# Optimization experiments

Hardware: AMD Instinct MI355X
Metric: run time of the kernel (lower is better)

Reference implementation:

```python
import jax, jax.numpy as jnp
import numpy as np

H, D_MODEL, D_K, D_V = 16, 1024, 64, 64
IS_DECODE = True


def setup_inputs() -> dict:
    key = jax.random.key(0)
    ks = jax.random.split(key, 6)
    N, L = 4, 2048
    x = jax.random.normal(ks[0], (N, L, D_MODEL), dtype=jnp.float32)
    masked_info = jnp.ones((N, L), dtype=jnp.float32)  # 1 = valid, 0 = pad
    s = 1.0 / np.sqrt(D_MODEL)
    WQ = jax.random.normal(ks[1], (H, D_MODEL, D_K), dtype=jnp.float32) * s
    WK = jax.random.normal(ks[2], (H, D_MODEL, D_K), dtype=jnp.float32) * s
    WV = jax.random.normal(ks[3], (H, D_MODEL, D_V), dtype=jnp.float32) * s
    WO = jax.random.normal(ks[4], (H * D_V, D_MODEL), dtype=jnp.float32) * s
    return {"x": x, "masked_info": masked_info, "WQ": WQ, "WK": WK, "WV": WV, "WO": WO}


def reference(x, masked_info, WQ, WK, WV, WO):
    N, L, _ = x.shape
    scaler = jnp.sqrt(jnp.array(D_K, dtype=x.dtype))
    # per-head projections, batched over heads: [H, N, L, d]
    q = jnp.einsum('nld,hdk->hnlk', x, WQ)
    k = jnp.einsum('nld,hdk->hnlk', x, WK)
    v = jnp.einsum('nld,hdv->hnlv', x, WV)
    scores = jnp.einsum('hnlk,hnmk->hnlm', q, k) / scaler  # [H, N, L, L]
    # outer-product padding mask: True where masked out
    pad_mask = (masked_info[:, :, None] * masked_info[:, None, :]) == 0  # [N, L, L]
    if IS_DECODE:
        causal = jnp.triu(jnp.ones((L, L), dtype=bool), k=1)
        pad_mask = pad_mask | causal[None, :, :]
    scores = jnp.where(pad_mask[None], -jnp.inf, scores)
    attn = jax.nn.softmax(scores, axis=-1)
    attn = jnp.nan_to_num(attn, nan=0.0)  # rows fully masked -> 0
    out_h = jnp.einsum('hnlm,hnmv->hnlv', attn, v)  # [H, N, L, d_v]
    # concat heads along last dim in head order: [N, L, H*d_v]
    concat = jnp.transpose(out_h, (1, 2, 0, 3)).reshape(N, L, H * D_V)
    return concat @ WO
```

## Files before the change

kernel.cpp:

```cpp
#include <hip/hip_runtime.h>
#include <hip/hip_bf16.h>


typedef unsigned short ushort_t;
typedef __bf16 bf16x8 __attribute__((ext_vector_type(8)));
typedef float  f32x4  __attribute__((ext_vector_type(4)));
typedef unsigned short us4 __attribute__((ext_vector_type(4)));
typedef short s16x4 __attribute__((ext_vector_type(4)));

__device__ __forceinline__ ushort_t f2bf(float f) {
    union { float f; unsigned u; } a; a.f = f;
    unsigned r = a.u + 0x7fffu + ((a.u >> 16) & 1u);
    return (ushort_t)(r >> 16);
}

__device__ __forceinline__ void gload16(const ushort_t* g, ushort_t* l) {
    __builtin_amdgcn_global_load_lds(
        (const __attribute__((address_space(1))) void*)g,
        (__attribute__((address_space(3))) void*)l, 16, 0, 0);
}

__global__ __launch_bounds__(256) void cvt_f32_bf16(const float* __restrict__ in,
                                                    ushort_t* __restrict__ out, int n4) {
    int i = blockIdx.x * 256 + threadIdx.x;
    if (i >= n4) return;
    float4 v = reinterpret_cast<const float4*>(in)[i];
    us4 o;
    o[0] = f2bf(v.x); o[1] = f2bf(v.y); o[2] = f2bf(v.z); o[3] = f2bf(v.w);
    reinterpret_cast<us4*>(out)[i] = o;
}

__global__ __launch_bounds__(256) void cvt_transpose32(const float* __restrict__ in,
                                                       ushort_t* __restrict__ out,
                                                       int R, int C) {
    const int b = blockIdx.z;
    const int c0 = blockIdx.x * 32, r0 = blockIdx.y * 32;
    const int tx = threadIdx.x & 31, ty = threadIdx.x >> 5;
    __shared__ ushort_t t[32][33];
    const float* ip = in + ((size_t)b * R + r0) * C + c0;
    #pragma unroll
    for (int i = 0; i < 4; ++i)
        t[ty + 8 * i][tx] = f2bf(ip[(size_t)(ty + 8 * i) * C + tx]);
    __syncthreads();
    ushort_t* op = out + ((size_t)b * C + c0) * R + r0;
    #pragma unroll
    for (int i = 0; i < 4; ++i)
        op[(size_t)(ty + 8 * i) * R + tx] = t[tx][ty + 8 * i];
}

__global__ __launch_bounds__(256) void cvt_transpose_qkv(const float* __restrict__ WQ,
                                                         const float* __restrict__ WK,
                                                         const float* __restrict__ WV,
                                                         ushort_t* __restrict__ out) {
    const int z = blockIdx.z;
    const float* in = (z < 16) ? WQ : (z < 32) ? WK : WV;
    const int b = z & 15;
    const int c0 = blockIdx.x * 32, r0 = blockIdx.y * 32;
    const int tx = threadIdx.x & 31, ty = threadIdx.x >> 5;
    __shared__ ushort_t t[32][33];
    const float* ip = in + ((size_t)b * 1024 + r0) * 64 + c0;
    #pragma unroll
    for (int i = 0; i < 4; ++i)
        t[ty + 8 * i][tx] = f2bf(ip[(size_t)(ty + 8 * i) * 64 + tx]);
    __syncthreads();
    ushort_t* op = out + (size_t)z * 65536 + (size_t)c0 * 1024 + r0;
    #pragma unroll
    for (int i = 0; i < 4; ++i)
        op[(size_t)(ty + 8 * i) * 1024 + tx] = t[tx][ty + 8 * i];
}

template<int MODE>
__global__ __launch_bounds__(256, 2)
void gemm_bt(const ushort_t* __restrict__ Ag, const ushort_t* __restrict__ BT,
             void* __restrict__ Cout, float scale) {
    const int bm = blockIdx.x, by = blockIdx.y;
    const int tid = threadIdx.x;
    const int w = tid >> 6, lane = tid & 63;
    const int wr = w >> 1, wc = w & 1;
    const int g = lane >> 4, c = lane & 15;
    const int m0 = bm * 128;
    const ushort_t* Bbase = BT + (size_t)by * 131072;

    __shared__ __align__(16) ushort_t As[128 * 64];
    __shared__ __align__(16) ushort_t Bs[128 * 64];

    f32x4 acc[4][4];
    #pragma unroll
    for (int i = 0; i < 4; ++i)
        #pragma unroll
        for (int j = 0; j < 4; ++j) acc[i][j] = (f32x4){0.f, 0.f, 0.f, 0.f};

    const int rsub = (w << 3) + (lane >> 3);
    const int s8   = lane & 7;

    for (int t = 0; t < 16; ++t) {
        const int k0 = t * 64;
        #pragma unroll
        for (int is = 0; is < 4; ++is) {
            const int row = is * 32 + rsub;
            const int sg  = (s8 ^ (row & 7)) << 3;
            gload16(Ag + (size_t)(m0 + row) * 1024 + k0 + sg, &As[is * 2048 + w * 512]);
            gload16(Bbase + (size_t)row * 1024 + k0 + sg,     &Bs[is * 2048 + w * 512]);
        }
        __syncthreads();
        #pragma unroll
        for (int kk = 0; kk < 2; ++kk) {
            bf16x8 af[4], bfr[4];
            #pragma unroll
            for (int mf = 0; mf < 4; ++mf) {
                const int row = wr * 64 + mf * 16 + c;
                const int slot = (kk * 4 + g) ^ (row & 7);
                af[mf] = *reinterpret_cast<const bf16x8*>(&As[row * 64 + slot * 8]);
            }
            #pragma unroll
            for (int nf = 0; nf < 4; ++nf) {
                const int row = wc * 64 + nf * 16 + c;
                const int slot = (kk * 4 + g) ^ (row & 7);
                bfr[nf] = *reinterpret_cast<const bf16x8*>(&Bs[row * 64 + slot * 8]);
            }
            __builtin_amdgcn_s_setprio(1);
            #pragma unroll
            for (int mf = 0; mf < 4; ++mf)
                #pragma unroll
                for (int nf = 0; nf < 4; ++nf)
                    acc[mf][nf] = __builtin_amdgcn_mfma_f32_16x16x32_bf16(
                        af[mf], bfr[nf], acc[mf][nf], 0, 0, 0);
            __builtin_amdgcn_s_setprio(0);
        }
        __syncthreads();
    }

    #pragma unroll
    for (int mf = 0; mf < 4; ++mf) {
        const int mbase = m0 + wr * 64 + mf * 16 + g * 4;
        #pragma unroll
        for (int nf = 0; nf < 4; ++nf) {
            const int colG = wc * 64 + nf * 16 + c;
            if (MODE == 3) {
                const int s  = by * 2 + (colG >> 6);
                const int c2 = colG & 63;
                ushort_t* o = (ushort_t*)Cout + (size_t)s * 524288;
                if (s < 32) {
                    const float scl = (s < 16) ? scale : 1.0f;
                    #pragma unroll
                    for (int r = 0; r < 4; ++r)
                        o[(size_t)(mbase + r) * 64 + c2] = f2bf(acc[mf][nf][r] * scl);
                } else {
                    us4 pk;
                    #pragma unroll
                    for (int r = 0; r < 4; ++r) pk[r] = f2bf(acc[mf][nf][r]);
                    const int nIdx = mbase >> 11, l = mbase & 2047;
                    *reinterpret_cast<us4*>(
                        &o[(size_t)nIdx * 131072 + (size_t)c2 * 2048 + l]) = pk;
                }
            } else {
                float* o = (float*)Cout;
                #pragma unroll
                for (int r = 0; r < 4; ++r)
                    o[(size_t)(mbase + r) * 1024 + by * 128 + colG] = acc[mf][nf][r];
            }
        }
    }
}

__global__ __launch_bounds__(256, 4)
void attn_kernel(const ushort_t* __restrict__ qb, const ushort_t* __restrict__ kb,
                 const ushort_t* __restrict__ vtb, const float* __restrict__ mi,
                 ushort_t* __restrict__ cat) {
    const int bx = blockIdx.x;
    const int n = blockIdx.y, h = blockIdx.z;
    const int tid = threadIdx.x;
    const int w = tid >> 6, lane = tid & 63;
    const int g = lane >> 4, c = lane & 15;
    const int qblkA = bx, qblkB = 31 - bx;
    const int q0A = qblkA * 64 + w * 16;
    const int q0B = qblkB * 64 + w * 16;

    const ushort_t* qhn = qb  + (size_t)h * 524288 + (size_t)n * 131072;
    const ushort_t* khn = kb  + (size_t)h * 524288 + (size_t)n * 131072;
    const ushort_t* vhn = vtb + (size_t)h * 524288 + (size_t)n * 131072;
    const float*    mrow = mi + (size_t)n * 2048;

    __shared__ __align__(16) ushort_t Ks[2][64 * 64];
    __shared__ __align__(16) ushort_t Vs[2][64 * 64];

    const int rsub = (w << 3) + (lane >> 3);
    const int s8   = lane & 7;

    auto stage = [&](int jb, int b) {
        const int kbase = jb * 64;
        #pragma unroll
        for (int is = 0; is < 2; ++is) {
            const int row = is * 32 + rsub;
            const int sg  = (s8 ^ (row & 7)) << 3;
            gload16(khn + (size_t)(kbase + row) * 64 + sg, &Ks[b][is * 2048 + w * 512]);
            gload16(vhn + (size_t)row * 2048 + kbase + sg, &Vs[b][is * 2048 + w * 512]);
        }
    };

    bf16x8 qfA[2], qfB[2];
    {
        const ushort_t* qa = qhn + (size_t)(q0A + c) * 64 + g * 8;
        const ushort_t* qb2 = qhn + (size_t)(q0B + c) * 64 + g * 8;
        qfA[0] = *reinterpret_cast<const bf16x8*>(qa);
        qfA[1] = *reinterpret_cast<const bf16x8*>(qa + 32);
        qfB[0] = *reinterpret_cast<const bf16x8*>(qb2);
        qfB[1] = *reinterpret_cast<const bf16x8*>(qb2 + 32);
    }
    const float mqA = mrow[q0A + c];
    const float mqB = mrow[q0B + c];

    float mrunA = -1e30f, lrunA = 0.f, mrunB = -1e30f, lrunB = 0.f;
    f32x4 accA[4], accB[4];
    #pragma unroll
    for (int i = 0; i < 4; ++i) {
        accA[i] = (f32x4){0.f, 0.f, 0.f, 0.f};
        accB[i] = (f32x4){0.f, 0.f, 0.f, 0.f};
    }

    stage(0, 0);
    __syncthreads();
    int buf = 0;

    for (int j = 0; j <= qblkB; ++j) {
        if (j < qblkB) stage(j + 1, buf ^ 1);
        const int kbase = j * 64;
        f32x4 bias[4];
        #pragma unroll
        for (int nf = 0; nf < 4; ++nf) {
            float4 mk = *reinterpret_cast<const float4*>(&mrow[kbase + nf * 16 + g * 4]);
            bias[nf][0] = (mk.x == 0.f) ? -1e30f : 0.f;
            bias[nf][1] = (mk.y == 0.f) ? -1e30f : 0.f;
            bias[nf][2] = (mk.z == 0.f) ? -1e30f : 0.f;
            bias[nf][3] = (mk.w == 0.f) ? -1e30f : 0.f;
        }

        auto do_pass = [&](const bf16x8* qf, f32x4* acc, float& mrun, float& lrun,
                           int q0, bool diag) {
            f32x4 s[4];
            #pragma unroll
            for (int nf = 0; nf < 4; ++nf) s[nf] = (f32x4){0.f, 0.f, 0.f, 0.f};
            __builtin_amdgcn_s_setprio(1);
            #pragma unroll
            for (int kk = 0; kk < 2; ++kk)
                #pragma unroll
                for (int nf = 0; nf < 4; ++nf) {
                    const int row  = nf * 16 + c;
                    const int byte = row * 128 + (((kk * 4 + g) ^ (c & 7)) << 4);
                    bf16x8 kf = *reinterpret_cast<const bf16x8*>(
                        reinterpret_cast<const char*>(&Ks[buf][0]) + byte);
                    s[nf] = __builtin_amdgcn_mfma_f32_16x16x32_bf16(
                        kf, qf[kk], s[nf], 0, 0, 0);
                }
            __builtin_amdgcn_s_setprio(0);
            #pragma unroll
            for (int nf = 0; nf < 4; ++nf) s[nf] += bias[nf];
            if (diag) {
                const int qrow = q0 + c;
                #pragma unroll
                for (int nf = 0; nf < 4; ++nf)
                    #pragma unroll
                    for (int r = 0; r < 4; ++r)
                        if (kbase + nf * 16 + g * 4 + r > qrow) s[nf][r] = -1e30f;
            }
            float m01[4], m23[4];
            #pragma unroll
            for (int r = 0; r < 4; ++r) {
                m01[r] = fmaxf(s[0][r], s[1][r]);
                m23[r] = fmaxf(s[2][r], s[3][r]);
            }
            const float mtl = fmaxf(fmaxf(fmaxf(m01[0], m01[1]), fmaxf(m01[2], m01[3])),
                                    fmaxf(fmaxf(m23[0], m23[1]), fmaxf(m23[2], m23[3])));
            if (!__all(mtl - mrun <= 8.0f)) {
                float mt = fmaxf(mtl, __shfl_xor(mtl, 16));
                mt = fmaxf(mt, __shfl_xor(mt, 32));
                const float mnew = fmaxf(mrun, mt);
                const float sc = __builtin_amdgcn_exp2f(mrun - mnew);
                #pragma unroll
                for (int nfd = 0; nfd < 4; ++nfd)
                    #pragma unroll
                    for (int r = 0; r < 4; ++r) acc[nfd][r] *= sc;
                lrun *= sc;
                mrun = mnew;
            }
            float rs = 0.f;
            union { unsigned u[2]; s16x4 v; } pb[4];
            #pragma unroll
            for (int nf = 0; nf < 4; ++nf) {
                const float p0 = __builtin_amdgcn_exp2f(s[nf][0] - mrun);
                const float p1 = __builtin_amdgcn_exp2f(s[nf][1] - mrun);
                const float p2 = __builtin_amdgcn_exp2f(s[nf][2] - mrun);
                const float p3 = __builtin_amdgcn_exp2f(s[nf][3] - mrun);
                rs += (p0 + p1) + (p2 + p3);
                asm("v_cvt_pk_bf16_f32 %0, %1, %2" : "=v"(pb[nf].u[0]) : "v"(p0), "v"(p1));
                asm("v_cvt_pk_bf16_f32 %0, %1, %2" : "=v"(pb[nf].u[1]) : "v"(p2), "v"(p3));
            }
            lrun += rs;
            __builtin_amdgcn_s_setprio(1);
            #pragma unroll
            for (int kk = 0; kk < 4; ++kk)
                #pragma unroll
                for (int nfd = 0; nfd < 4; ++nfd) {
                    const int row   = nfd * 16 + c;
                    const int chunk = (kk * 2 + (g >> 1)) ^ (c & 7);
                    const int byt   = row * 128 + (chunk << 4) + (g & 1) * 8;
                    s16x4 vf = *reinterpret_cast<const s16x4*>(
                        reinterpret_cast<const char*>(&Vs[buf][0]) + byt);
                    acc[nfd] = __builtin_amdgcn_mfma_f32_16x16x16bf16_1k(
                        vf, pb[kk].v, acc[nfd], 0, 0, 0);
                }
            __builtin_amdgcn_s_setprio(0);
        };

        if (j <= qblkA) do_pass(qfA, accA, mrunA, lrunA, q0A, j == qblkA);
        do_pass(qfB, accB, mrunB, lrunB, q0B, j == qblkB);

        __syncthreads();
        buf ^= 1;
    }

    auto epi = [&](const f32x4* acc, float mrun, float lrun, float mq, int q0) {
        float lt = lrun;
        lt += __shfl_xor(lt, 16);
        lt += __shfl_xor(lt, 32);
        const float inv = (mq != 0.f && mrun > -1e29f && lt > 0.f)
                              ? (1.0f / lt) : 0.f;
        const size_t base = (size_t)(n * 2048 + q0 + c) * 1024 + h * 64;
        #pragma unroll
        for (int nfd = 0; nfd < 4; ++nfd) {
            us4 pk;
            #pragma unroll
            for (int r = 0; r < 4; ++r) pk[r] = f2bf(acc[nfd][r] * inv);
            *reinterpret_cast<us4*>(&cat[base + nfd * 16 + g * 4]) = pk;
        }
    };
    epi(accA, mrunA, lrunA, mqA, q0A);
    epi(accB, mrunB, lrunB, mqB, q0B);
}

extern "C" void kernel_launch(void* const* d_in, const int* in_sizes, int n_in,
                              void* d_out, int out_size, void* d_ws, size_t ws_size,
                              hipStream_t stream) {
    const float* x  = (const float*)d_in[0];
    const float* mi = (const float*)d_in[1];
    const float* WQ = (const float*)d_in[2];
    const float* WK = (const float*)d_in[3];
    const float* WV = (const float*)d_in[4];
    const float* WO = (const float*)d_in[5];
    float* out = (float*)d_out;

    ushort_t* ws  = (ushort_t*)d_ws;
    ushort_t* xb  = ws;
    ushort_t* wqt = xb  + 8388608;
    ushort_t* wot = wqt + 3145728;
    ushort_t* qb  = wot + 1048576;
    ushort_t* kb  = qb  + 8388608;
    ushort_t* vtb = kb  + 8388608;
    ushort_t* cat = xb;

    cvt_f32_bf16<<<8192, 256, 0, stream>>>(x, xb, 2097152);
    {
        dim3 gt(2, 32, 48);
        cvt_transpose_qkv<<<gt, 256, 0, stream>>>(WQ, WK, WV, wqt);
        dim3 go(32, 32, 1);
        cvt_transpose32<<<go, 256, 0, stream>>>(WO, wot, 1024, 1024);
    }

    dim3 g1(64, 24);
    gemm_bt<3><<<g1, 256, 0, stream>>>(xb, wqt, qb, 0.18033688f);

    dim3 g2(16, 4, 16);
    attn_kernel<<<g2, 256, 0, stream>>>(qb, kb, vtb, mi, cat);

    dim3 g3(64, 8);
    gemm_bt<2><<<g3, 256, 0, stream>>>(cat, wot, out, 1.0f);
}
```

Before: 185.0 us.

## Replace paired causal query blocks with one block per workgroup, longest first

The attention kernel previously gave each workgroup two query blocks (bx and 31-bx) so every workgroup did the same amount of causal work. Now each workgroup handles a single query block, the grid doubles to 32 blocks in x, and blocks are numbered in reverse so the longest ones launch first. Launch bounds rise to 5 waves per SIMD since fewer registers are live. The aim is more parallelism and occupancy, at the cost of uneven per-workgroup work and reloading K/V tiles separately for each query block.

```diff
diff --git a/kernel.cpp b/kernel.cpp
--- a/kernel.cpp
+++ b/kernel.cpp
@@ -163,18 +163,16 @@
     }
 }
 
-__global__ __launch_bounds__(256, 4)
+__global__ __launch_bounds__(256, 5)
 void attn_kernel(const ushort_t* __restrict__ qb, const ushort_t* __restrict__ kb,
                  const ushort_t* __restrict__ vtb, const float* __restrict__ mi,
                  ushort_t* __restrict__ cat) {
-    const int bx = blockIdx.x;
+    const int qblk = 31 - blockIdx.x;
     const int n = blockIdx.y, h = blockIdx.z;
     const int tid = threadIdx.x;
     const int w = tid >> 6, lane = tid & 63;
     const int g = lane >> 4, c = lane & 15;
-    const int qblkA = bx, qblkB = 31 - bx;
-    const int q0A = qblkA * 64 + w * 16;
-    const int q0B = qblkB * 64 + w * 16;
+    const int q0 = qblk * 64 + w * 16;
 
     const ushort_t* qhn = qb  + (size_t)h * 524288 + (size_t)n * 131072;
     const ushort_t* khn = kb  + (size_t)h * 524288 + (size_t)n * 131072;
@@ -198,128 +196,125 @@
         }
     };
 
-    bf16x8 qfA[2], qfB[2];
+    bf16x8 qf[2];
     {
-        const ushort_t* qa = qhn + (size_t)(q0A + c) * 64 + g * 8;
-        const ushort_t* qb2 = qhn + (size_t)(q0B + c) * 64 + g * 8;
-        qfA[0] = *reinterpret_cast<const bf16x8*>(qa);
-        qfA[1] = *reinterpret_cast<const bf16x8*>(qa + 32);
-        qfB[0] = *reinterpret_cast<const bf16x8*>(qb2);
-        qfB[1] = *reinterpret_cast<const bf16x8*>(qb2 + 32);
-    }
-    const float mqA = mrow[q0A + c];
-    const float mqB = mrow[q0B + c];
-
-    float mrunA = -1e30f, lrunA = 0.f, mrunB = -1e30f, lrunB = 0.f;
-    f32x4 accA[4], accB[4];
-    #pragma unroll
-    for (int i = 0; i < 4; ++i) {
-        accA[i] = (f32x4){0.f, 0.f, 0.f, 0.f};
-        accB[i] = (f32x4){0.f, 0.f, 0.f, 0.f};
-    }
+        const ushort_t* qa = qhn + (size_t)(q0 + c) * 64 + g * 8;
+        qf[0] = *reinterpret_cast<const bf16x8*>(qa);
+        qf[1] = *reinterpret_cast<const bf16x8*>(qa + 32);
+    }
+    const float mq = mrow[q0 + c];
+
+    float mrun = -1e30f, lrun = 0.f;
+    f32x4 acc[4];
+    #pragma unroll
+    for (int i = 0; i < 4; ++i) acc[i] = (f32x4){0.f, 0.f, 0.f, 0.f};
 
     stage(0, 0);
     __syncthreads();
     int buf = 0;
 
-    for (int j = 0; j <= qblkB; ++j) {
-        if (j < qblkB) stage(j + 1, buf ^ 1);
+    for (int j = 0; j <= qblk; ++j) {
+        if (j < qblk) stage(j + 1, buf ^ 1);
         const int kbase = j * 64;
-        f32x4 bias[4];
+        const bool diag = (j == qblk);
+        f32x4 bias;
+        {
+            float4 mk0 = *reinterpret_cast<const float4*>(&mrow[kbase + g * 4]);
+            bias[0] = (mk0.x == 0.f) ? -1e30f : 0.f;
+            bias[1] = (mk0.y == 0.f) ? -1e30f : 0.f;
+            bias[2] = (mk0.z == 0.f) ? -1e30f : 0.f;
+            bias[3] = (mk0.w == 0.f) ? -1e30f : 0.f;
+        }
+        f32x4 bias2[3];
+        #pragma unroll
+        for (int nf = 1; nf < 4; ++nf) {
+            float4 mk = *reinterpret_cast<const float4*>(&mrow[kbase + nf * 16 + g * 4]);
+            bias2[nf - 1][0] = (mk.x == 0.f) ? -1e30f : 0.f;
+            bias2[nf - 1][1] = (mk.y == 0.f) ? -1e30f : 0.f;
+            bias2[nf - 1][2] = (mk.z == 0.f) ? -1e30f : 0.f;
+            bias2[nf - 1][3] = (mk.w == 0.f) ? -1e30f : 0.f;
+        }
+
+        f32x4 s[4];
+        #pragma unroll
+        for (int nf = 0; nf < 4; ++nf) s[nf] = (f32x4){0.f, 0.f, 0.f, 0.f};
+        __builtin_amdgcn_s_setprio(1);
+        #pragma unroll
+        for (int kk = 0; kk < 2; ++kk)
+            #pragma unroll
+            for (int nf = 0; nf < 4; ++nf) {
+                const int row  = nf * 16 + c;
+                const int byte = row * 128 + (((kk * 4 + g) ^ (c & 7)) << 4);
+                bf16x8 kf = *reinterpret_cast<const bf16x8*>(
+                    reinterpret_cast<const char*>(&Ks[buf][0]) + byte);
+                s[nf] = __builtin_amdgcn_mfma_f32_16x16x32_bf16(
+                    kf, qf[kk], s[nf], 0, 0, 0);
+            }
+        __builtin_amdgcn_s_setprio(0);
+        s[0] += bias;
+        #pragma unroll
+        for (int nf = 1; nf < 4; ++nf) s[nf] += bias2[nf - 1];
+        if (diag) {
+            const int qrow = q0 + c;
+            #pragma unroll
+            for (int nf = 0; nf < 4; ++nf)
+                #pragma unroll
+                for (int r = 0; r < 4; ++r)
+                    if (kbase + nf * 16 + g * 4 + r > qrow) s[nf][r] = -1e30f;
+        }
+        float m01[4], m23[4];
+        #pragma unroll
+        for (int r = 0; r < 4; ++r) {
+            m01[r] = fmaxf(s[0][r], s[1][r]);
+            m23[r] = fmaxf(s[2][r], s[3][r]);
+        }
+        const float mtl = fmaxf(fmaxf(fmaxf(m01[0], m01[1]), fmaxf(m01[2], m01[3])),
+                                fmaxf(fmaxf(m23[0], m23[1]), fmaxf(m23[2], m23[3])));
+        if (!__all(mtl - mrun <= 8.0f)) {
+            float mt = fmaxf(mtl, __shfl_xor(mtl, 16));
+            mt = fmaxf(mt, __shfl_xor(mt, 32));
+            const float mnew = fmaxf(mrun, mt);
+            const float sc = __builtin_amdgcn_exp2f(mrun - mnew);
+            #pragma unroll
+            for (int nfd = 0; nfd < 4; ++nfd)
+                #pragma unroll
+                for (int r = 0; r < 4; ++r) acc[nfd][r] *= sc;
+            lrun *= sc;
+            mrun = mnew;
+        }
+        float rs = 0.f;
+        union { unsigned u[2]; s16x4 v; } pb[4];
         #pragma unroll
         for (int nf = 0; nf < 4; ++nf) {
-            float4 mk = *reinterpret_cast<const float4*>(&mrow[kbase + nf * 16 + g * 4]);
-            bias[nf][0] = (mk.x == 0.f) ? -1e30f : 0.f;
-            bias[nf][1] = (mk.y == 0.f) ? -1e30f : 0.f;
-            bias[nf][2] = (mk.z == 0.f) ? -1e30f : 0.f;
-            bias[nf][3] = (mk.w == 0.f) ? -1e30f : 0.f;
-        }
-
-        auto do_pass = [&](const bf16x8* qf, f32x4* acc, float& mrun, float& lrun,
-                           int q0, bool diag) {
-            f32x4 s[4];
-            #pragma unroll
-            for (int nf = 0; nf < 4; ++nf) s[nf] = (f32x4){0.f, 0.f, 0.f, 0.f};
-            __builtin_amdgcn_s_setprio(1);
-            #pragma unroll
-            for (int kk = 0; kk < 2; ++kk)
-                #pragma unroll
-                for (int nf = 0; nf < 4; ++nf) {
-                    const int row  = nf * 16 + c;
-                    const int byte = row * 128 + (((kk * 4 + g) ^ (c & 7)) << 4);
-                    bf16x8 kf = *reinterpret_cast<const bf16x8*>(
-                        reinterpret_cast<const char*>(&Ks[buf][0]) + byte);
-                    s[nf] = __builtin_amdgcn_mfma_f32_16x16x32_bf16(
-                        kf, qf[kk], s[nf], 0, 0, 0);
-                }
-            __builtin_amdgcn_s_setprio(0);
-            #pragma unroll
-            for (int nf = 0; nf < 4; ++nf) s[nf] += bias[nf];
-            if (diag) {
-                const int qrow = q0 + c;
-                #pragma unroll
-                for (int nf = 0; nf < 4; ++nf)
-                    #pragma unroll
-                    for (int r = 0; r < 4; ++r)
-                        if (kbase + nf * 16 + g * 4 + r > qrow) s[nf][r] = -1e30f;
-            }
-            float m01[4], m23[4];
-            #pragma unroll
-            for (int r = 0; r < 4; ++r) {
-                m01[r] = fmaxf(s[0][r], s[1][r]);
-                m23[r] = fmaxf(s[2][r], s[3][r]);
-            }
-            const float mtl = fmaxf(fmaxf(fmaxf(m01[0], m01[1]), fmaxf(m01[2], m01[3])),
-                                    fmaxf(fmaxf(m23[0], m23[1]), fmaxf(m23[2], m23[3])));
-            if (!__all(mtl - mrun <= 8.0f)) {
-                float mt = fmaxf(mtl, __shfl_xor(mtl, 16));
-                mt = fmaxf(mt, __shfl_xor(mt, 32));
-                const float mnew = fmaxf(mrun, mt);
-                const float sc = __builtin_amdgcn_exp2f(mrun - mnew);
-                #pragma unroll
-                for (int nfd = 0; nfd < 4; ++nfd)
-                    #pragma unroll
-                    for (int r = 0; r < 4; ++r) acc[nfd][r] *= sc;
-                lrun *= sc;
-                mrun = mnew;
-            }
-            float rs = 0.f;
-            union { unsigned u[2]; s16x4 v; } pb[4];
-            #pragma unroll
-            for (int nf = 0; nf < 4; ++nf) {
-                const float p0 = __builtin_amdgcn_exp2f(s[nf][0] - mrun);
-                const float p1 = __builtin_amdgcn_exp2f(s[nf][1] - mrun);
-                const float p2 = __builtin_amdgcn_exp2f(s[nf][2] - mrun);
-                const float p3 = __builtin_amdgcn_exp2f(s[nf][3] - mrun);
-                rs += (p0 + p1) + (p2 + p3);
-                asm("v_cvt_pk_bf16_f32 %0, %1, %2" : "=v"(pb[nf].u[0]) : "v"(p0), "v"(p1));
-                asm("v_cvt_pk_bf16_f32 %0, %1, %2" : "=v"(pb[nf].u[1]) : "v"(p2), "v"(p3));
-            }
-            lrun += rs;
-            __builtin_amdgcn_s_setprio(1);
-            #pragma unroll
-            for (int kk = 0; kk < 4; ++kk)
-                #pragma unroll
-                for (int nfd = 0; nfd < 4; ++nfd) {
-                    const int row   = nfd * 16 + c;
-                    const int chunk = (kk * 2 + (g >> 1)) ^ (c & 7);
-                    const int byt   = row * 128 + (chunk << 4) + (g & 1) * 8;
-                    s16x4 vf = *reinterpret_cast<const s16x4*>(
-                        reinterpret_cast<const char*>(&Vs[buf][0]) + byt);
-                    acc[nfd] = __builtin_amdgcn_mfma_f32_16x16x16bf16_1k(
-                        vf, pb[kk].v, acc[nfd], 0, 0, 0);
-                }
-            __builtin_amdgcn_s_setprio(0);
-        };
-
-        if (j <= qblkA) do_pass(qfA, accA, mrunA, lrunA, q0A, j == qblkA);
-        do_pass(qfB, accB, mrunB, lrunB, q0B, j == qblkB);
+            const float p0 = __builtin_amdgcn_exp2f(s[nf][0] - mrun);
+            const float p1 = __builtin_amdgcn_exp2f(s[nf][1] - mrun);
+            const float p2 = __builtin_amdgcn_exp2f(s[nf][2] - mrun);
+            const float p3 = __builtin_amdgcn_exp2f(s[nf][3] - mrun);
+            rs += (p0 + p1) + (p2 + p3);
+            asm("v_cvt_pk_bf16_f32 %0, %1, %2" : "=v"(pb[nf].u[0]) : "v"(p0), "v"(p1));
+            asm("v_cvt_pk_bf16_f32 %0, %1, %2" : "=v"(pb[nf].u[1]) : "v"(p2), "v"(p3));
+        }
+        lrun += rs;
+        __builtin_amdgcn_s_setprio(1);
+        #pragma unroll
+        for (int kk = 0; kk < 4; ++kk)
+            #pragma unroll
+            for (int nfd = 0; nfd < 4; ++nfd) {
+                const int row   = nfd * 16 + c;
+                const int chunk = (kk * 2 + (g >> 1)) ^ (c & 7);
+                const int byt   = row * 128 + (chunk << 4) + (g & 1) * 8;
+                s16x4 vf = *reinterpret_cast<const s16x4*>(
+                    reinterpret_cast<const char*>(&Vs[buf][0]) + byt);
+                acc[nfd] = __builtin_amdgcn_mfma_f32_16x16x16bf16_1k(
+                    vf, pb[kk].v, acc[nfd], 0, 0, 0);
+            }
+        __builtin_amdgcn_s_setprio(0);
 
         __syncthreads();
         buf ^= 1;
     }
 
-    auto epi = [&](const f32x4* acc, float mrun, float lrun, float mq, int q0) {
+    {
         float lt = lrun;
         lt += __shfl_xor(lt, 16);
         lt += __shfl_xor(lt, 32);
@@ -333,9 +328,7 @@
             for (int r = 0; r < 4; ++r) pk[r] = f2bf(acc[nfd][r] * inv);
             *reinterpret_cast<us4*>(&cat[base + nfd * 16 + g * 4]) = pk;
         }
-    };
-    epi(accA, mrunA, lrunA, mqA, q0A);
-    epi(accB, mrunB, lrunB, mqB, q0B);
+    }
 }
 
 extern "C" void kernel_launch(void* const* d_in, const int* in_sizes, int n_in,
@@ -369,7 +362,7 @@
     dim3 g1(64, 24);
     gemm_bt<3><<<g1, 256, 0, stream>>>(xb, wqt, qb, 0.18033688f);
 
-    dim3 g2(16, 4, 16);
+    dim3 g2(32, 4, 16);
     attn_kernel<<<g2, 256, 0, stream>>>(qb, kb, vtb, mi, cat);
 
     dim3 g3(64, 8);
```

Result: slower. 231.7 us (+25.2%).
